# Kernel tuning notes

Hardware: AMD Instinct MI355X
Metric: run time of the kernel (lower is better)

Reference implementation:

```python
import jax, jax.numpy as jnp
import numpy as np

B, N, DIM = 2, 2048, 512
HEADS, DIM_HEAD = 8, 64
TIME_DIM = 512
EPS = 1e-5
NEG = 1e6


def setup_inputs() -> dict:
    key = jax.random.key(0)
    ks = jax.random.split(key, 8)
    return {
        "x": jax.random.normal(ks[0], (B, N, DIM), jnp.float32),
        "time": jax.random.normal(ks[1], (B, 1, TIME_DIM), jnp.float32),
        "attn_bias": jax.random.normal(ks[2], (B, HEADS, N, N), jnp.float32) * 0.1,
        "seq_mask": jnp.ones((B, N), jnp.float32),
        "gamma": jnp.ones((DIM,), jnp.float32),
        "w_time": jax.random.normal(ks[3], (2 * DIM, TIME_DIM), jnp.float32) * 0.02,
        "b_time": jax.random.normal(ks[4], (2 * DIM,), jnp.float32) * 0.02,
        "w_q": jax.random.normal(ks[5], (HEADS * DIM_HEAD, DIM), jnp.float32) * 0.02,
        "w_kv": jax.random.normal(ks[6], (2 * HEADS * DIM_HEAD, DIM), jnp.float32) * 0.02,
        "w_out": jax.random.normal(ks[7], (DIM, HEADS * DIM_HEAD), jnp.float32) * 0.02,
    }


def reference(x, time, attn_bias, seq_mask, gamma, w_time, b_time, w_q, w_kv, w_out):
    # NOTE: context = x BEFORE norm/time-cond/mask (faithful to original ordering)
    context = x
    # LayerNorm (beta buffer is zeros)
    mu = jnp.mean(x, axis=-1, keepdims=True)
    var = jnp.mean(jnp.square(x - mu), axis=-1, keepdims=True)
    xn = (x - mu) * jax.lax.rsqrt(var + EPS) * gamma
    # FiLM time conditioning: SiLU -> Linear -> (scale, shift)
    t = jax.nn.silu(time) @ w_time.T + b_time            # [b,1,2*dim]
    sc, sh = jnp.split(t, 2, axis=-1)
    xn = xn * (sc + 1.0) + sh
    # sequence mask on queries' input
    xn = xn * seq_mask[..., None]
    # projections
    q = (xn @ w_q.T).reshape(B, N, HEADS, DIM_HEAD).transpose(0, 2, 1, 3)   # b h n d
    kv = context @ w_kv.T                                                    # [b,n,2*h*d]
    k, v = jnp.split(kv, 2, axis=-1)
    k = k.reshape(B, N, HEADS, DIM_HEAD).transpose(0, 2, 1, 3)
    v = v.reshape(B, N, HEADS, DIM_HEAD).transpose(0, 2, 1, 3)
    q = q * (DIM_HEAD ** -0.5)
    # attention scores with additive bias and pairwise seq mask
    sim = jnp.einsum('bhid,bhjd->bhij', q, k) + attn_bias
    pair_mask = seq_mask[:, None, :, None] * seq_mask[:, None, None, :]      # b 1 i j
    sim = sim - (1.0 - pair_mask) * NEG
    attn = jax.nn.softmax(sim, axis=-1)
    out = jnp.einsum('bhij,bhjd->bhid', attn, v)
    out = out.transpose(0, 2, 1, 3).reshape(B, N, HEADS * DIM_HEAD)
    out = out @ w_out.T
    out = out * seq_mask[..., None]
    return out
```

## Files before the change

### kernel.cpp

```cpp
#include <hip/hip_runtime.h>
#include <stdint.h>


using s16x8 = __attribute__((ext_vector_type(8))) short;
using f32x4 = __attribute__((ext_vector_type(4))) float;
using u16x4 = __attribute__((ext_vector_type(4))) unsigned short;
using u32x2 = __attribute__((ext_vector_type(2))) unsigned int;

#define EPSV 1e-5f
#define NEGV 1e6f
#define L2E  1.44269504088896341f
#define QSCL 0.18033688011112043f

__device__ __forceinline__ unsigned short f2bf(float f) {
    unsigned int u = __float_as_uint(f);
    u += 0x7FFFu + ((u >> 16) & 1u);
    return (unsigned short)(u >> 16);
}
__device__ __forceinline__ float bf2f(unsigned short s) {
    return __uint_as_float((unsigned int)s << 16);
}

__device__ __forceinline__ void gl_lds16(const void* g, void* l) {
    __builtin_amdgcn_global_load_lds((const __attribute__((address_space(1))) void*)g,
                                     (__attribute__((address_space(3))) void*)l, 16, 0, 0);
}

__device__ __forceinline__ f32x4 mfma_bf16(s16x8 a, s16x8 b, f32x4 c) {
    return __builtin_amdgcn_mfma_f32_16x16x32_bf16(a, b, c, 0, 0, 0);
}

__global__ void k_pt(const float* __restrict__ w_q, const float* __restrict__ w_kv,
                     const float* __restrict__ w_out,
                     const float* __restrict__ timev, const float* __restrict__ w_time,
                     const float* __restrict__ b_time,
                     unsigned short* __restrict__ wq, unsigned short* __restrict__ wkv,
                     unsigned short* __restrict__ wo_h, unsigned short* __restrict__ wo_l,
                     float* __restrict__ tc) {
    if (blockIdx.x < 4096) {
        int idx = blockIdx.x * 256 + threadIdx.x;
        if (idx < 262144) {
            wq[idx] = f2bf(w_q[idx]);
        } else if (idx < 786432) {
            int i = idx - 262144;
            wkv[i] = f2bf(w_kv[i]);
        } else {
            int i = idx - 786432;
            float v = w_out[i];
            unsigned short h = f2bf(v);
            wo_h[i] = h;
            wo_l[i] = f2bf(v - bf2f(h));
        }
    } else {
        int bid = blockIdx.x - 4096;
        int wid = threadIdx.x >> 6, lane = threadIdx.x & 63;
        int b = bid >> 8;
        int j = (bid & 255) * 4 + wid;
        const float* tv = timev + b * 512;
        const float* wr = w_time + (size_t)j * 512;
        float acc = 0.f;
#pragma unroll
        for (int i = 0; i < 8; ++i) {
            int k = i * 64 + lane;
            float t = tv[k];
            float s = t / (1.f + __expf(-t));
            acc += s * wr[k];
        }
#pragma unroll
        for (int m = 32; m >= 1; m >>= 1) acc += __shfl_xor(acc, m);
        if (lane == 0) tc[b * 1024 + j] = acc + b_time[j];
    }
}

__global__ void k_lnfilm(const float* __restrict__ x, const float* __restrict__ gamma,
                         const float* __restrict__ seq_mask, const float* __restrict__ tc,
                         unsigned short* __restrict__ xbf, unsigned short* __restrict__ xnbf) {
    int row = blockIdx.x * 4 + (threadIdx.x >> 6);
    int lane = threadIdx.x & 63;
    int b = row >> 11;
    const float* xr = x + (size_t)row * 512 + lane * 8;
    f32x4 x0 = *(const f32x4*)(xr);
    f32x4 x1 = *(const f32x4*)(xr + 4);
    float s = (x0[0] + x0[1]) + (x0[2] + x0[3]) + (x1[0] + x1[1]) + (x1[2] + x1[3]);
    float sq = x0[0] * x0[0];
    sq = __builtin_fmaf(x0[1], x0[1], sq);
    sq = __builtin_fmaf(x0[2], x0[2], sq);
    sq = __builtin_fmaf(x0[3], x0[3], sq);
    sq = __builtin_fmaf(x1[0], x1[0], sq);
    sq = __builtin_fmaf(x1[1], x1[1], sq);
    sq = __builtin_fmaf(x1[2], x1[2], sq);
    sq = __builtin_fmaf(x1[3], x1[3], sq);
#pragma unroll
    for (int m = 32; m >= 1; m >>= 1) { s += __shfl_xor(s, m); sq += __shfl_xor(sq, m); }
    float mu = s * (1.f / 512.f);
    float var = sq * (1.f / 512.f) - mu * mu;
    float rs = rsqrtf(var + EPSV);
    float qm = seq_mask[row];
    int j = lane * 8;
    const float* scb = tc + b * 1024 + j;
    f32x4 g0 = *(const f32x4*)(gamma + j);
    f32x4 g1 = *(const f32x4*)(gamma + j + 4);
    f32x4 c0 = *(const f32x4*)(scb);
    f32x4 c1 = *(const f32x4*)(scb + 4);
    f32x4 h0 = *(const f32x4*)(scb + 512);
    f32x4 h1 = *(const f32x4*)(scb + 516);
    u16x4 n0, n1, v0, v1;
#pragma unroll
    for (int e = 0; e < 4; ++e) {
        float o0 = ((x0[e] - mu) * rs * g0[e]) * (c0[e] + 1.f) + h0[e];
        float o1 = ((x1[e] - mu) * rs * g1[e]) * (c1[e] + 1.f) + h1[e];
        n0[e] = f2bf(o0 * qm);
        n1[e] = f2bf(o1 * qm);
        v0[e] = f2bf(x0[e]);
        v1[e] = f2bf(x1[e]);
    }
    size_t base = (size_t)row * 512 + j;
    *(u16x4*)(xnbf + base)     = n0;
    *(u16x4*)(xnbf + base + 4) = n1;
    *(u16x4*)(xbf + base)      = v0;
    *(u16x4*)(xbf + base + 4)  = v1;
}

__launch_bounds__(256)
__global__ void k_gemm2(const unsigned short* __restrict__ xnbf,
                        const unsigned short* __restrict__ xbf,
                        const unsigned short* __restrict__ wq,
                        const unsigned short* __restrict__ wkv,
                        unsigned short* __restrict__ qb,
                        unsigned short* __restrict__ kb,
                        unsigned short* __restrict__ vtb) {
    __shared__ unsigned short a_t[128 * 64];
    __shared__ unsigned short b_t[128 * 64];
    int tid = threadIdx.x, lane = tid & 63, wid = tid >> 6;
    int lc = lane & 15, lq = lane >> 4;
    int wr = wid >> 1, wc = wid & 1;
    bool isQ = blockIdx.y < 4;
    int m0 = blockIdx.x * 128;
    int n0 = (isQ ? blockIdx.y : blockIdx.y - 4) * 128;
    const unsigned short* A = isQ ? xnbf : xbf;
    const unsigned short* W = isQ ? wq : wkv;
    f32x4 acc[4][4];
#pragma unroll
    for (int i = 0; i < 4; ++i)
#pragma unroll
        for (int jn = 0; jn < 4; ++jn)
#pragma unroll
            for (int e = 0; e < 4; ++e) acc[i][jn][e] = 0.f;
    const unsigned short* Ab = A + (size_t)m0 * 512;
    const unsigned short* Wb = W + (size_t)n0 * 512;
    int wbase = wid * 64;
    for (int kt = 0; kt < 8; ++kt) {
        __syncthreads();
#pragma unroll
        for (int i = 0; i < 4; ++i) {
            int p = i * 256 + wbase + lane;
            int row = p >> 3, ls = (p & 7) ^ (row & 7);
            gl_lds16(Ab + (size_t)row * 512 + kt * 64 + ls * 8, a_t + (i * 256 + wbase) * 8);
            gl_lds16(Wb + (size_t)row * 512 + kt * 64 + ls * 8, b_t + (i * 256 + wbase) * 8);
        }
        __syncthreads();
        s16x8 af[4][2], bw[4][2];
        const char* ab = (const char*)a_t;
        const char* bb = (const char*)b_t;
#pragma unroll
        for (int mf = 0; mf < 4; ++mf) {
            int row = wr * 64 + mf * 16 + lc;
            int key = (row & 7) << 4;
            af[mf][0] = *(const s16x8*)(ab + row * 128 + ((lq * 16) ^ key));
            af[mf][1] = *(const s16x8*)(ab + row * 128 + ((64 + lq * 16) ^ key));
        }
#pragma unroll
        for (int nf = 0; nf < 4; ++nf) {
            int row = wc * 64 + nf * 16 + lc;
            int key = (row & 7) << 4;
            bw[nf][0] = *(const s16x8*)(bb + row * 128 + ((lq * 16) ^ key));
            bw[nf][1] = *(const s16x8*)(bb + row * 128 + ((64 + lq * 16) ^ key));
        }
#pragma unroll
        for (int mf = 0; mf < 4; ++mf)
#pragma unroll
            for (int nf = 0; nf < 4; ++nf) {
                acc[mf][nf] = mfma_bf16(af[mf][0], bw[nf][0], acc[mf][nf]);
                acc[mf][nf] = mfma_bf16(af[mf][1], bw[nf][1], acc[mf][nf]);
            }
    }
#pragma unroll
    for (int mf = 0; mf < 4; ++mf)
#pragma unroll
        for (int nf = 0; nf < 4; ++nf) {
            int grow0 = m0 + wr * 64 + mf * 16 + lq * 4;
            int gcol = n0 + wc * 64 + nf * 16 + lc;
            int b = grow0 >> 11, nb = grow0 & 2047;
            if (isQ) {
                int h = gcol >> 6, d = gcol & 63;
#pragma unroll
                for (int r = 0; r < 4; ++r)
                    qb[((size_t)((b * 8 + h) * 2048 + nb + r)) * 64 + d] =
                        f2bf(acc[mf][nf][r] * QSCL);
            } else if (gcol < 512) {
                int h = gcol >> 6, d = gcol & 63;
#pragma unroll
                for (int r = 0; r < 4; ++r)
                    kb[((size_t)((b * 8 + h) * 2048 + nb + r)) * 64 + d] = f2bf(acc[mf][nf][r]);
            } else {
                int jj = gcol & 511;
                int h = jj >> 6, d = jj & 63;
                u16x4 vv;
#pragma unroll
                for (int r = 0; r < 4; ++r) vv[r] = f2bf(acc[mf][nf][r]);
                *(u16x4*)(vtb + ((size_t)((b * 8 + h) * 64 + d)) * 2048 + nb) = vv;
            }
        }
}

__launch_bounds__(256)
__global__ void k_attn(const unsigned short* __restrict__ qg, const unsigned short* __restrict__ kg,
                       const unsigned short* __restrict__ vt, const float* __restrict__ bias,
                       const float* __restrict__ seq_mask,
                       unsigned short* __restrict__ ah, unsigned short* __restrict__ al) {
    __shared__ unsigned short k_ring[2][64 * 64];
    __shared__ unsigned short v_ring[2][64 * 64];
    __shared__ __align__(16) char b_ring[2][16384];
    __shared__ __align__(16) char scr[4][2048];
    __shared__ __align__(16) float km_lds[2048];

    int tid = threadIdx.x, lane = tid & 63, w = tid >> 6;
    int lc = lane & 15, lq = lane >> 4;

    int lin = blockIdx.x;
    int vid = (lin & 7) * 64 + (lin >> 3);
    int bh = vid >> 5;
    int q0 = (vid & 31) * 64 + w * 16;
    int b = bh >> 3, h = bh & 7;

    const unsigned short* qbase = qg + ((size_t)bh * 2048 + q0) * 64;
    s16x8 aq0 = *(const s16x8*)(qbase + lc * 64 + lq * 8);
    s16x8 aq1 = *(const s16x8*)(qbase + lc * 64 + 32 + lq * 8);

    const unsigned short* kb = kg + (size_t)bh * 2048 * 64;
    const unsigned short* vt0 = vt + (size_t)bh * 64 * 2048;
    const float* bqb = bias + ((size_t)bh * 2048 + q0) * 2048;
    const float* sk = seq_mask + b * 2048;
    const float NEG2 = NEGV * L2E;
    float qm_ = seq_mask[b * 2048 + q0 + lc];

    char* pw = &scr[w][0];
    int swz = (lc & 7) << 4;
    int brow = lane >> 4, bchk = lane & 15;

    float mst = -1e30f, lst = 0.f;
    f32x4 acc[4];
#pragma unroll
    for (int df = 0; df < 4; ++df)
#pragma unroll
        for (int e = 0; e < 4; ++e) acc[df][e] = 0.f;

    auto issue_k = [&](int tile, int slot) {
#pragma unroll
        for (int i = 0; i < 2; ++i) {
            int off = w * 2048 + i * 1024 + lane * 16;
            int row = off >> 7;
            int cc = ((off >> 4) & 7) ^ (row & 7);
            gl_lds16(kb + ((size_t)tile * 64 + row) * 64 + cc * 8,
                     (char*)k_ring[slot] + w * 2048 + i * 1024);
        }
    };
    auto issue_vt = [&](int tile, int slot) {
#pragma unroll
        for (int i = 0; i < 2; ++i) {
            int off = w * 2048 + i * 1024 + lane * 16;
            int row = off >> 7;
            int cc = ((off >> 4) & 7) ^ (row & 7);
            gl_lds16(vt0 + (size_t)row * 2048 + tile * 64 + cc * 8,
                     (char*)v_ring[slot] + w * 2048 + i * 1024);
        }
    };
    auto issue_b = [&](int tile, int slot) {
#pragma unroll
        for (int i = 0; i < 4; ++i) {
            int row = i * 4 + brow;
            int kc = bchk ^ (row & 7);
            gl_lds16(bqb + (size_t)row * 2048 + tile * 64 + kc * 4,
                     (char*)b_ring[slot] + w * 4096 + i * 1024);
        }
    };

    issue_k(0, 0);
    issue_vt(0, 0);
    issue_b(0, 0);
#pragma unroll
    for (int i = 0; i < 2; ++i)
        gl_lds16(sk + w * 512 + i * 256 + lane * 4,
                 (char*)km_lds + w * 2048 + i * 1024);
    __builtin_amdgcn_sched_barrier(0);
    asm volatile("s_waitcnt vmcnt(0)");
    __builtin_amdgcn_s_barrier();
    __builtin_amdgcn_sched_barrier(0);

    auto iter = [&](int kt, int par) {
        const int slot_nxt = par ^ 1;

        {
            int tk = (kt + 1 < 32) ? kt + 1 : 31;
            issue_k(tk, slot_nxt);
            issue_vt(tk, slot_nxt);
            __builtin_amdgcn_sched_barrier(0);
            issue_b(tk, slot_nxt);
        }
        __builtin_amdgcn_sched_barrier(0);

        const char* klds = (const char*)k_ring[par];
        f32x4 sv[4];
        __builtin_amdgcn_s_setprio(1);
#pragma unroll
        for (int nf = 0; nf < 4; ++nf) {
            int row = nf * 16 + lc;
            s16x8 b0 = *(const s16x8*)(klds + row * 128 + ((lq * 16) ^ swz));
            s16x8 b1 = *(const s16x8*)(klds + row * 128 + ((64 + lq * 16) ^ swz));
            f32x4 z;
            z[0] = 0.f; z[1] = 0.f; z[2] = 0.f; z[3] = 0.f;
            z = mfma_bf16(b0, aq0, z);
            z = mfma_bf16(b1, aq1, z);
            sv[nf] = z;
        }
        __builtin_amdgcn_s_setprio(0);

        __builtin_amdgcn_sched_barrier(0);
        asm volatile("s_waitcnt vmcnt(8)");
        __builtin_amdgcn_sched_barrier(0);
        const char* bws = (const char*)b_ring[par] + w * 4096;
        f32x4 bv[4], km[4];
#pragma unroll
        for (int nf = 0; nf < 4; ++nf) {
            bv[nf] = *(const f32x4*)(bws + lc * 256 + ((((nf << 2) + lq) ^ (lc & 7)) << 4));
            km[nf] = *(const f32x4*)((const char*)km_lds + kt * 256 + nf * 64 + lq * 16);
        }

#pragma unroll
        for (int nf = 0; nf < 4; ++nf) {
#pragma unroll
            for (int e = 0; e < 4; ++e) {
                float pen = __builtin_fmaf(km[nf][e], qm_, -1.0f) * NEG2;
                sv[nf][e] = __builtin_fmaf(bv[nf][e], L2E, sv[nf][e]) + pen;
            }
        }

        f32x4 m4 = sv[0];
#pragma unroll
        for (int nf = 1; nf < 4; ++nf)
#pragma unroll
            for (int e = 0; e < 4; ++e) m4[e] = fmaxf(m4[e], sv[nf][e]);
        float mx = fmaxf(fmaxf(m4[0], m4[1]), fmaxf(m4[2], m4[3]));
        mx = fmaxf(mx, __shfl_xor(mx, 16));
        mx = fmaxf(mx, __shfl_xor(mx, 32));
        if (!__all(mx <= mst + 11.54f)) {
            float mn = fmaxf(mst, mx);
            float scl = __builtin_amdgcn_exp2f(mst - mn);
            lst *= scl;
#pragma unroll
            for (int df = 0; df < 4; ++df)
#pragma unroll
                for (int e = 0; e < 4; ++e) acc[df][e] *= scl;
            mst = mn;
        }
        float rsum = 0.f;
#pragma unroll
        for (int nf = 0; nf < 4; ++nf) {
            f32x4 p;
#pragma unroll
            for (int e = 0; e < 4; ++e) {
                p[e] = __builtin_amdgcn_exp2f(sv[nf][e] - mst);
                rsum += p[e];
            }
            unsigned int pk01, pk23;
            asm("v_cvt_pk_bf16_f32 %0, %1, %2" : "=v"(pk01) : "v"(p[0]), "v"(p[1]));
            asm("v_cvt_pk_bf16_f32 %0, %1, %2" : "=v"(pk23) : "v"(p[2]), "v"(p[3]));
            u32x2 pkv;
            pkv[0] = pk01; pkv[1] = pk23;
            *(u32x2*)(pw + lc * 128 + ((nf * 32 + lq * 8) ^ swz)) = pkv;
        }
        rsum += __shfl_xor(rsum, 16);
        rsum += __shfl_xor(rsum, 32);
        lst += rsum;

        __builtin_amdgcn_sched_barrier(0);
        asm volatile("s_waitcnt lgkmcnt(0)");
        __builtin_amdgcn_sched_barrier(0);

        s16x8 ap0 = *(const s16x8*)(pw + lc * 128 + ((lq * 16) ^ swz));
        s16x8 ap1 = *(const s16x8*)(pw + lc * 128 + ((64 + lq * 16) ^ swz));
        const char* vlds = (const char*)v_ring[par];
        __builtin_amdgcn_s_setprio(1);
#pragma unroll
        for (int df = 0; df < 4; ++df) {
            int row = df * 16 + lc;
            int key = (row & 7) << 4;
            s16x8 av0 = *(const s16x8*)(vlds + row * 128 + ((lq * 16) ^ key));
            s16x8 av1 = *(const s16x8*)(vlds + row * 128 + ((64 + lq * 16) ^ key));
            acc[df] = mfma_bf16(av0, ap0, acc[df]);
            acc[df] = mfma_bf16(av1, ap1, acc[df]);
        }
        __builtin_amdgcn_s_setprio(0);

        __builtin_amdgcn_sched_barrier(0);
        asm volatile("s_waitcnt vmcnt(4) lgkmcnt(0)");
        __builtin_amdgcn_s_barrier();
        __builtin_amdgcn_sched_barrier(0);
    };

    for (int t = 0; t < 16; ++t) {
        iter(2 * t,     0);
        iter(2 * t + 1, 1);
    }
    asm volatile("s_waitcnt vmcnt(0)");

    float inv = 1.f / lst;
    size_t rowb = ((size_t)(b * 2048 + q0 + lc)) * 512 + h * 64;
#pragma unroll
    for (int df = 0; df < 4; ++df) {
        u16x4 hi, lo;
#pragma unroll
        for (int r = 0; r < 4; ++r) {
            float o = acc[df][r] * inv;
            unsigned short hb = f2bf(o);
            hi[r] = hb;
            lo[r] = f2bf(o - bf2f(hb));
        }
        *(u16x4*)(ah + rowb + df * 16 + lq * 4) = hi;
        *(u16x4*)(al + rowb + df * 16 + lq * 4) = lo;
    }
}

__launch_bounds__(256)
__global__ void k_gemm_out(const unsigned short* __restrict__ Ah, const unsigned short* __restrict__ Al,
                           const unsigned short* __restrict__ Wh, const unsigned short* __restrict__ Wl,
                           const float* __restrict__ seq_mask, float* __restrict__ out) {
    __shared__ unsigned short ah_t[64 * 32], al_t[64 * 32], bh_t[128 * 32], bl_t[128 * 32];
    int tid = threadIdx.x, lane = tid & 63, wid = tid >> 6;
    int lc = lane & 15, lq = lane >> 4;
    int wc = wid;
    int m0 = blockIdx.x * 64, n0 = blockIdx.y * 128;
    f32x4 acc[4][2];
#pragma unroll
    for (int i = 0; i < 4; ++i)
#pragma unroll
        for (int jn = 0; jn < 2; ++jn)
#pragma unroll
            for (int e = 0; e < 4; ++e) acc[i][jn][e] = 0.f;
    int wbase = wid * 64;
    for (int kt = 0; kt < 16; ++kt) {
        __syncthreads();
        {
            int p = wbase + lane;
            int row = p >> 2, ls = (p & 3) ^ (row & 3);
            size_t asrc = (size_t)(m0 + row) * 512 + kt * 32 + ls * 8;
            gl_lds16(Ah + asrc, ah_t + (wbase + lane - lane) * 8 + wbase * 8 - wbase * 8 + p * 8);
        }
        {
            int p = wbase + lane;
            int row = p >> 2, ls = (p & 3) ^ (row & 3);
            size_t asrc = (size_t)(m0 + row) * 512 + kt * 32 + ls * 8;
            gl_lds16(Al + asrc, al_t + wbase * 8);
            gl_lds16(Ah + asrc, ah_t + wbase * 8);
        }
#pragma unroll
        for (int i = 0; i < 2; ++i) {
            int p = i * 256 + wbase + lane;
            int row = p >> 2, ls = (p & 3) ^ (row & 3);
            size_t bsrc = (size_t)(n0 + row) * 512 + kt * 32 + ls * 8;
            gl_lds16(Wh + bsrc, bh_t + (i * 256 + wbase) * 8);
            gl_lds16(Wl + bsrc, bl_t + (i * 256 + wbase) * 8);
        }
        __syncthreads();
        s16x8 fah[4], fal[4], fbh[2], fbl[2];
#pragma unroll
        for (int mf = 0; mf < 4; ++mf) {
            int row = mf * 16 + lc;
            int off = row * 64 + ((lq * 16) ^ ((row & 3) << 4));
            fah[mf] = *(const s16x8*)((const char*)ah_t + off);
            fal[mf] = *(const s16x8*)((const char*)al_t + off);
        }
#pragma unroll
        for (int nf = 0; nf < 2; ++nf) {
            int row = wc * 32 + nf * 16 + lc;
            int off = row * 64 + ((lq * 16) ^ ((row & 3) << 4));
            fbh[nf] = *(const s16x8*)((const char*)bh_t + off);
            fbl[nf] = *(const s16x8*)((const char*)bl_t + off);
        }
#pragma unroll
        for (int mf = 0; mf < 4; ++mf)
#pragma unroll
            for (int nf = 0; nf < 2; ++nf) {
                acc[mf][nf] = mfma_bf16(fah[mf], fbh[nf], acc[mf][nf]);
                acc[mf][nf] = mfma_bf16(fah[mf], fbl[nf], acc[mf][nf]);
                acc[mf][nf] = mfma_bf16(fal[mf], fbh[nf], acc[mf][nf]);
            }
    }
#pragma unroll
    for (int mf = 0; mf < 4; ++mf)
#pragma unroll
        for (int nf = 0; nf < 2; ++nf)
#pragma unroll
            for (int r = 0; r < 4; ++r) {
                int grow = m0 + mf * 16 + lq * 4 + r;
                int gcol = n0 + wc * 32 + nf * 16 + lc;
                out[(size_t)grow * 512 + gcol] = acc[mf][nf][r] * seq_mask[grow];
            }
}

extern "C" void kernel_launch(void* const* d_in, const int* in_sizes, int n_in,
                              void* d_out, int out_size, void* d_ws, size_t ws_size,
                              hipStream_t stream) {
    const float* x         = (const float*)d_in[0];
    const float* timev     = (const float*)d_in[1];
    const float* attn_bias = (const float*)d_in[2];
    const float* seq_mask  = (const float*)d_in[3];
    const float* gamma     = (const float*)d_in[4];
    const float* w_time    = (const float*)d_in[5];
    const float* b_time    = (const float*)d_in[6];
    const float* w_q       = (const float*)d_in[7];
    const float* w_kv      = (const float*)d_in[8];
    const float* w_out     = (const float*)d_in[9];
    float* out = (float*)d_out;

    char* ws = (char*)d_ws;
    size_t off = 0;
    auto alloc = [&](size_t bytes) {
        char* p = ws + off;
        off += (bytes + 255) & ~(size_t)255;
        return p;
    };
    float*          tc   = (float*)alloc(2048 * 4);
    unsigned short* wq   = (unsigned short*)alloc(262144 * 2);
    unsigned short* wkv  = (unsigned short*)alloc(524288 * 2);
    unsigned short* wo_h = (unsigned short*)alloc(262144 * 2);
    unsigned short* wo_l = (unsigned short*)alloc(262144 * 2);
    unsigned short* xbf  = (unsigned short*)alloc(2097152 * 2);
    unsigned short* xnbf = (unsigned short*)alloc(2097152 * 2);
    unsigned short* qb   = (unsigned short*)alloc(2097152 * 2);
    unsigned short* kb   = (unsigned short*)alloc(2097152 * 2);
    unsigned short* vtb  = (unsigned short*)alloc(2097152 * 2);
    unsigned short* ahh  = (unsigned short*)alloc(2097152 * 2);
    unsigned short* all_ = (unsigned short*)alloc(2097152 * 2);

    k_pt<<<4608, 256, 0, stream>>>(w_q, w_kv, w_out, timev, w_time, b_time,
                                   wq, wkv, wo_h, wo_l, tc);
    k_lnfilm<<<1024, 256, 0, stream>>>(x, gamma, seq_mask, tc, xbf, xnbf);
    k_gemm2<<<dim3(32, 12), 256, 0, stream>>>(xnbf, xbf, wq, wkv, qb, kb, vtb);
    k_attn<<<512, 256, 0, stream>>>(qb, kb, vtb, attn_bias, seq_mask, ahh, all_);
    k_gemm_out<<<dim3(64, 4), 256, 0, stream>>>(ahh, all_, wo_h, wo_l, seq_mask, out);
}
```

Before: 123.3 us.

## Load K, V and key mask directly from global, dropping LDS staging rings

The attention kernel no longer stages K, V^T and the key sequence mask through double-buffered LDS rings. Each wave now reads its K and V fragments and mask values straight from global memory into registers. This removes the block-wide barrier and the async LDS copies, leaving only the per-wave bias ring with an adjusted vmcnt wait. The trade-off is that all four waves fetch the same K/V tiles redundantly through the cache, and those loads are no longer prefetched, so their latency sits in front of the MFMAs. The output-projection GEMM also stops issuing a duplicate load of the Ah tile.

```diff
diff --git a/kernel.cpp b/kernel.cpp
--- a/kernel.cpp
+++ b/kernel.cpp
@@ -218,11 +218,8 @@
                        const unsigned short* __restrict__ vt, const float* __restrict__ bias,
                        const float* __restrict__ seq_mask,
                        unsigned short* __restrict__ ah, unsigned short* __restrict__ al) {
-    __shared__ unsigned short k_ring[2][64 * 64];
-    __shared__ unsigned short v_ring[2][64 * 64];
     __shared__ __align__(16) char b_ring[2][16384];
     __shared__ __align__(16) char scr[4][2048];
-    __shared__ __align__(16) float km_lds[2048];
 
     int tid = threadIdx.x, lane = tid & 63, w = tid >> 6;
     int lc = lane & 15, lq = lane >> 4;
@@ -255,26 +252,6 @@
 #pragma unroll
         for (int e = 0; e < 4; ++e) acc[df][e] = 0.f;
 
-    auto issue_k = [&](int tile, int slot) {
-#pragma unroll
-        for (int i = 0; i < 2; ++i) {
-            int off = w * 2048 + i * 1024 + lane * 16;
-            int row = off >> 7;
-            int cc = ((off >> 4) & 7) ^ (row & 7);
-            gl_lds16(kb + ((size_t)tile * 64 + row) * 64 + cc * 8,
-                     (char*)k_ring[slot] + w * 2048 + i * 1024);
-        }
-    };
-    auto issue_vt = [&](int tile, int slot) {
-#pragma unroll
-        for (int i = 0; i < 2; ++i) {
-            int off = w * 2048 + i * 1024 + lane * 16;
-            int row = off >> 7;
-            int cc = ((off >> 4) & 7) ^ (row & 7);
-            gl_lds16(vt0 + (size_t)row * 2048 + tile * 64 + cc * 8,
-                     (char*)v_ring[slot] + w * 2048 + i * 1024);
-        }
-    };
     auto issue_b = [&](int tile, int slot) {
 #pragma unroll
         for (int i = 0; i < 4; ++i) {
@@ -285,16 +262,9 @@
         }
     };
 
-    issue_k(0, 0);
-    issue_vt(0, 0);
     issue_b(0, 0);
-#pragma unroll
-    for (int i = 0; i < 2; ++i)
-        gl_lds16(sk + w * 512 + i * 256 + lane * 4,
-                 (char*)km_lds + w * 2048 + i * 1024);
     __builtin_amdgcn_sched_barrier(0);
     asm volatile("s_waitcnt vmcnt(0)");
-    __builtin_amdgcn_s_barrier();
     __builtin_amdgcn_sched_barrier(0);
 
     auto iter = [&](int kt, int par) {
@@ -302,39 +272,39 @@
 
         {
             int tk = (kt + 1 < 32) ? kt + 1 : 31;
-            issue_k(tk, slot_nxt);
-            issue_vt(tk, slot_nxt);
-            __builtin_amdgcn_sched_barrier(0);
             issue_b(tk, slot_nxt);
         }
         __builtin_amdgcn_sched_barrier(0);
 
-        const char* klds = (const char*)k_ring[par];
+        f32x4 km[4];
+#pragma unroll
+        for (int nf = 0; nf < 4; ++nf)
+            km[nf] = *(const f32x4*)(sk + kt * 64 + nf * 16 + lq * 4);
+        __builtin_amdgcn_sched_barrier(0);
+
+        const unsigned short* kkt = kb + (size_t)kt * 64 * 64;
         f32x4 sv[4];
         __builtin_amdgcn_s_setprio(1);
 #pragma unroll
         for (int nf = 0; nf < 4; ++nf) {
-            int row = nf * 16 + lc;
-            s16x8 b0 = *(const s16x8*)(klds + row * 128 + ((lq * 16) ^ swz));
-            s16x8 b1 = *(const s16x8*)(klds + row * 128 + ((64 + lq * 16) ^ swz));
+            s16x8 k0 = *(const s16x8*)(kkt + (nf * 16 + lc) * 64 + lq * 8);
+            s16x8 k1 = *(const s16x8*)(kkt + (nf * 16 + lc) * 64 + 32 + lq * 8);
             f32x4 z;
             z[0] = 0.f; z[1] = 0.f; z[2] = 0.f; z[3] = 0.f;
-            z = mfma_bf16(b0, aq0, z);
-            z = mfma_bf16(b1, aq1, z);
+            z = mfma_bf16(k0, aq0, z);
+            z = mfma_bf16(k1, aq1, z);
             sv[nf] = z;
         }
         __builtin_amdgcn_s_setprio(0);
 
         __builtin_amdgcn_sched_barrier(0);
-        asm volatile("s_waitcnt vmcnt(8)");
+        asm volatile("s_waitcnt vmcnt(16)");
         __builtin_amdgcn_sched_barrier(0);
         const char* bws = (const char*)b_ring[par] + w * 4096;
-        f32x4 bv[4], km[4];
-#pragma unroll
-        for (int nf = 0; nf < 4; ++nf) {
+        f32x4 bv[4];
+#pragma unroll
+        for (int nf = 0; nf < 4; ++nf)
             bv[nf] = *(const f32x4*)(bws + lc * 256 + ((((nf << 2) + lq) ^ (lc & 7)) << 4));
-            km[nf] = *(const f32x4*)((const char*)km_lds + kt * 256 + nf * 64 + lq * 16);
-        }
 
 #pragma unroll
         for (int nf = 0; nf < 4; ++nf) {
@@ -389,23 +359,16 @@
 
         s16x8 ap0 = *(const s16x8*)(pw + lc * 128 + ((lq * 16) ^ swz));
         s16x8 ap1 = *(const s16x8*)(pw + lc * 128 + ((64 + lq * 16) ^ swz));
-        const char* vlds = (const char*)v_ring[par];
+        const unsigned short* vkt = vt0 + kt * 64;
         __builtin_amdgcn_s_setprio(1);
 #pragma unroll
         for (int df = 0; df < 4; ++df) {
-            int row = df * 16 + lc;
-            int key = (row & 7) << 4;
-            s16x8 av0 = *(const s16x8*)(vlds + row * 128 + ((lq * 16) ^ key));
-            s16x8 av1 = *(const s16x8*)(vlds + row * 128 + ((64 + lq * 16) ^ key));
-            acc[df] = mfma_bf16(av0, ap0, acc[df]);
-            acc[df] = mfma_bf16(av1, ap1, acc[df]);
+            s16x8 v0 = *(const s16x8*)(vkt + (size_t)(df * 16 + lc) * 2048 + lq * 8);
+            s16x8 v1 = *(const s16x8*)(vkt + (size_t)(df * 16 + lc) * 2048 + 32 + lq * 8);
+            acc[df] = mfma_bf16(v0, ap0, acc[df]);
+            acc[df] = mfma_bf16(v1, ap1, acc[df]);
         }
         __builtin_amdgcn_s_setprio(0);
-
-        __builtin_amdgcn_sched_barrier(0);
-        asm volatile("s_waitcnt vmcnt(4) lgkmcnt(0)");
-        __builtin_amdgcn_s_barrier();
-        __builtin_amdgcn_sched_barrier(0);
     };
 
     for (int t = 0; t < 16; ++t) {
@@ -454,14 +417,8 @@
             int p = wbase + lane;
             int row = p >> 2, ls = (p & 3) ^ (row & 3);
             size_t asrc = (size_t)(m0 + row) * 512 + kt * 32 + ls * 8;
-            gl_lds16(Ah + asrc, ah_t + (wbase + lane - lane) * 8 + wbase * 8 - wbase * 8 + p * 8);
-        }
-        {
-            int p = wbase + lane;
-            int row = p >> 2, ls = (p & 3) ^ (row & 3);
-            size_t asrc = (size_t)(m0 + row) * 512 + kt * 32 + ls * 8;
+            gl_lds16(Ah + asrc, ah_t + wbase * 8);
             gl_lds16(Al + asrc, al_t + wbase * 8);
-            gl_lds16(Ah + asrc, ah_t + wbase * 8);
         }
 #pragma unroll
         for (int i = 0; i < 2; ++i) {
```

Result: slower. 199.2 us (+61.5%).
